# Optimization experiments

Hardware: AMD Instinct MI355X
Metric: run time of the kernel (lower is better)

The kernel has to match this reference:

```python
import jax, jax.numpy as jnp
import numpy as np
from jax import lax

NUM_HEADS = 16
DIM = 1024
BATCH = 4
SEQ = 2048


def setup_inputs() -> dict:
    key = jax.random.key(0)
    ks = jax.random.split(key, 12)
    f32 = jnp.float32
    q = jax.random.normal(ks[0], (BATCH, SEQ, DIM), dtype=f32)
    k = jax.random.normal(ks[1], (BATCH, SEQ, DIM), dtype=f32)
    v = jax.random.normal(ks[2], (BATCH, SEQ, DIM), dtype=f32)
    lim = 1.0 / np.sqrt(DIM)  # nn.Linear default init range
    Wi = jax.random.uniform(ks[3], (DIM, DIM), minval=-lim, maxval=lim, dtype=f32)
    bi = jax.random.uniform(ks[4], (DIM,), minval=-lim, maxval=lim, dtype=f32)
    Wg = jax.random.uniform(ks[5], (DIM, DIM), minval=-lim, maxval=lim, dtype=f32)
    bg = jax.random.uniform(ks[6], (DIM,), minval=-lim, maxval=lim, dtype=f32)
    Wo = jax.random.uniform(ks[7], (DIM, DIM), minval=-lim, maxval=lim, dtype=f32)
    bo = jax.random.uniform(ks[8], (DIM,), minval=-lim, maxval=lim, dtype=f32)
    A = jax.random.normal(ks[9], (DIM, DIM), dtype=f32) * 0.1
    Bm = jax.random.normal(ks[10], (DIM, DIM), dtype=f32) * 0.1
    decay = jnp.full((1, NUM_HEADS, 1), 0.9, dtype=f32)
    return dict(q=q, k=k, v=v, Wi=Wi, bi=bi, Wg=Wg, bg=bg, A=A, Bm=Bm,
                Wo=Wo, bo=bo, decay=decay)


def reference(q, k, v, Wi, bi, Wg, bg, A, Bm, Wo, bo, decay):
    B, S, D = q.shape
    H = decay.shape[1]
    hd = D // H
    # time-major heads: [S, B, H, hd]
    qh = jnp.moveaxis(q.reshape(B, S, H, hd), 1, 0)
    kh = jnp.moveaxis(k.reshape(B, S, H, hd), 1, 0)
    vh = jnp.moveaxis(v.reshape(B, S, H, hd), 1, 0)

    def step(carry, xs):
        r, state = carry
        qt, kt, vt = xs
        r = decay * r + kt * vt                         # [B, H, hd]
        retained = (qt * r).reshape(B, D)               # [B, D]
        inp = retained @ Wi.T + bi
        gate = jax.nn.sigmoid(inp @ Wg.T + bg)
        blended = gate * state + (1.0 - gate) * inp
        state = jnp.tanh(blended @ A.T + inp @ Bm.T)
        out = state @ Wo.T + bo                         # [B, D]
        return (r, state), out

    r0 = jnp.zeros((B, H, hd), dtype=q.dtype)
    s0 = jnp.zeros((B, D), dtype=q.dtype)
    _, outs = lax.scan(step, (r0, s0), (qh, kh, vh))     # outs: [S, B, D]
    return jnp.moveaxis(outs, 0, 1)                      # [B, S, D]
```

## Files before the change

kernel.cpp:

```cpp
#include <hip/hip_runtime.h>
#include <hip/hip_bf16.h>
#include <math.h>

#define BATCH 4
#define SEQ   2048
#define DIM   1024
#define MROWS (SEQ*BATCH)
#define BIGN  ((size_t)MROWS*DIM)

__global__ __launch_bounds__(256) void scan_a(const float* __restrict__ K,
    const float* __restrict__ V, const float* __restrict__ dec_p,
    float* __restrict__ E)
{
  int id  = blockIdx.x*256 + threadIdx.x;
  int c   = id >> 12;
  int rem = id & 4095;
  int b   = rem >> 10;
  int dc  = rem & 1023;
  float dec = dec_p[dc >> 6];
  size_t base = ((size_t)b*SEQ + (size_t)c*32)*DIM + dc;
  float r = 0.f;
  #pragma unroll 4
  for (int i = 0; i < 32; ++i) {
    float kv = K[base + (size_t)i*DIM] * V[base + (size_t)i*DIM];
    r = fmaf(dec, r, kv);
  }
  E[(size_t)c*4096 + rem] = r;
}

__global__ __launch_bounds__(256) void scan_b(const float* __restrict__ E,
    const float* __restrict__ dec_p, float* __restrict__ carry)
{
  int id = blockIdx.x*256 + threadIdx.x;
  int dc = id & 1023;
  float dec = dec_p[dc >> 6];
  float d2 = dec*dec, d4 = d2*d2, d8 = d4*d4, d16 = d8*d8, d32 = d16*d16;
  float r = 0.f;
  #pragma unroll 1
  for (int c = 0; c < 64; ++c) {
    carry[(size_t)c*4096 + id] = r;
    r = fmaf(d32, r, E[(size_t)c*4096 + id]);
  }
}

__global__ __launch_bounds__(256) void scan_c(const float* __restrict__ Q,
    const float* __restrict__ K, const float* __restrict__ V,
    const float* __restrict__ dec_p, const float* __restrict__ carry,
    float* __restrict__ ret)
{
  int id  = blockIdx.x*256 + threadIdx.x;
  int c   = id >> 12;
  int rem = id & 4095;
  int b   = rem >> 10;
  int dc  = rem & 1023;
  float dec = dec_p[dc >> 6];
  size_t base = ((size_t)b*SEQ + (size_t)c*32)*DIM + dc;
  float r = carry[(size_t)c*4096 + rem];
  #pragma unroll 1
  for (int i = 0; i < 32; ++i) {
    int t = c*32 + i;
    float kv = K[base + (size_t)i*DIM] * V[base + (size_t)i*DIM];
    r = fmaf(dec, r, kv);
    ret[((size_t)t*BATCH + b)*DIM + dc] = Q[base + (size_t)i*DIM] * r;
  }
}

#define GM 64
#define GN 64
#define GK 32
#define LDA 68

template<int MODE>
__global__ __launch_bounds__(256) void gemm_k(
    const float* __restrict__ X, const float* __restrict__ W,
    const float* __restrict__ bias, float* __restrict__ C,
    const float* __restrict__ inp, float* __restrict__ u_out,
    float* __restrict__ outf)
{
  __shared__ float Xs[GK][LDA];
  __shared__ float Ws[GK][LDA];
  const int tid = threadIdx.x;
  const int m0 = blockIdx.y * GM;
  const int n0 = blockIdx.x * GN;
  const int tx = tid & 15, ty = tid >> 4;
  float acc[4][4] = {};
  #pragma unroll 1
  for (int kb = 0; kb < DIM; kb += GK) {
    #pragma unroll
    for (int h = 0; h < 2; ++h) {
      int idx = tid + h*256;
      int row = idx >> 3;
      int kc  = (idx & 7) << 2;
      float4 xv = *(const float4*)(X + (size_t)(m0+row)*DIM + kb + kc);
      Xs[kc+0][row] = xv.x; Xs[kc+1][row] = xv.y;
      Xs[kc+2][row] = xv.z; Xs[kc+3][row] = xv.w;
      float4 wv = *(const float4*)(W + (size_t)(n0+row)*DIM + kb + kc);
      Ws[kc+0][row] = wv.x; Ws[kc+1][row] = wv.y;
      Ws[kc+2][row] = wv.z; Ws[kc+3][row] = wv.w;
    }
    __syncthreads();
    #pragma unroll
    for (int kk = 0; kk < GK; ++kk) {
      float4 a = *(const float4*)&Xs[kk][ty << 2];
      float4 w = *(const float4*)&Ws[kk][tx << 2];
      float av[4] = {a.x, a.y, a.z, a.w};
      float wv[4] = {w.x, w.y, w.z, w.w};
      #pragma unroll
      for (int i = 0; i < 4; ++i)
        #pragma unroll
        for (int j = 0; j < 4; ++j)
          acc[i][j] = fmaf(av[i], wv[j], acc[i][j]);
    }
    __syncthreads();
  }
  float bj[4];
  #pragma unroll
  for (int j = 0; j < 4; ++j)
    bj[j] = (MODE == 0 || MODE == 1 || MODE == 3) ? bias[n0 + (tx<<2) + j] : 0.f;
  #pragma unroll
  for (int i = 0; i < 4; ++i) {
    int m = m0 + (ty<<2) + i;
    #pragma unroll
    for (int j = 0; j < 4; ++j) {
      int n = n0 + (tx<<2) + j;
      size_t off = (size_t)m*DIM + n;
      float vv = acc[i][j] + bj[j];
      if (MODE == 2) vv += C[off];
      if (MODE == 1) {
        float gv = 1.f/(1.f + expf(-vv));
        C[off] = gv;
        u_out[off] = (1.f - gv) * inp[off];
      } else if (MODE == 3) {
        outf[((size_t)(m & 3)*SEQ + (size_t)(m >> 2))*DIM + n] = vv;
      } else {
        C[off] = vv;
      }
    }
  }
}

#define RBLK 64

__global__ __launch_bounds__(512, 2) void recur_k(
    const float* __restrict__ A, const float* __restrict__ g,
    const float* __restrict__ dpre, float* __restrict__ s,
    unsigned long long* __restrict__ sf)
{
  __shared__ __align__(16) float xs[8*132 + 4];
  const int tid = threadIdx.x;
  const int w   = tid >> 6;
  const int ln  = tid & 63;
  const int b   = blockIdx.x >> 4;
  const int blk = blockIdx.x & 15;
  const int row = blk*64 + w*8 + (ln >> 3);
  const int ks  = ln & 7;

  const size_t slotstride = (size_t)BATCH*DIM;
  unsigned long long* sfb = sf + (size_t)b*DIM;

  float4 areg[32];
  #pragma unroll
  for (int j = 0; j < 32; ++j)
    areg[j] = *(const float4*)(A + (size_t)row*DIM + ks*128 + 4*j);

  const int xoff = (tid >> 6)*132 + ((2*tid) & 127);

  #pragma unroll 1
  for (int t = 0; t < SEQ; ++t) {
    float2 gv = *(const float2*)(g + ((size_t)t*4 + b)*DIM + 2*tid);
    float dval = (ks == 0) ? dpre[((size_t)t*4 + b)*DIM + row] : 0.f;

    float acc0 = 0.f, acc1 = 0.f, acc2 = 0.f, acc3 = 0.f;
    if (t > 0) {
      unsigned long long* p0 = sfb + (size_t)((t-1)&1)*slotstride + 2*tid;
      const unsigned want = (unsigned)t;
      union { unsigned long long u; unsigned ui[2]; float f[2]; } a0, a1;
      int guard = 0;
      for (;;) {
        a0.u = __hip_atomic_load(p0,     __ATOMIC_RELAXED,
                                 __HIP_MEMORY_SCOPE_AGENT);
        a1.u = __hip_atomic_load(p0 + 1, __ATOMIC_RELAXED,
                                 __HIP_MEMORY_SCOPE_AGENT);
        if ((a0.ui[1] == want && a1.ui[1] == want) || ++guard > (1 << 25))
          break;
      }

      *(float2*)(xs + xoff) = make_float2(gv.x * a0.f[0], gv.y * a1.f[0]);
      __syncthreads();

      const float* xb = xs + ks*132;
      #pragma unroll
      for (int j = 0; j < 32; j += 4) {
        float4 x0 = *(const float4*)(xb + 4*j);
        float4 x1 = *(const float4*)(xb + 4*j + 4);
        float4 x2 = *(const float4*)(xb + 4*j + 8);
        float4 x3 = *(const float4*)(xb + 4*j + 12);
        acc0 = fmaf(areg[j+0].x, x0.x, fmaf(areg[j+0].y, x0.y,
               fmaf(areg[j+0].z, x0.z, fmaf(areg[j+0].w, x0.w, acc0))));
        acc1 = fmaf(areg[j+1].x, x1.x, fmaf(areg[j+1].y, x1.y,
               fmaf(areg[j+1].z, x1.z, fmaf(areg[j+1].w, x1.w, acc1))));
        acc2 = fmaf(areg[j+2].x, x2.x, fmaf(areg[j+2].y, x2.y,
               fmaf(areg[j+2].z, x2.z, fmaf(areg[j+2].w, x2.w, acc2))));
        acc3 = fmaf(areg[j+3].x, x3.x, fmaf(areg[j+3].y, x3.y,
               fmaf(areg[j+3].z, x3.z, fmaf(areg[j+3].w, x3.w, acc3))));
      }
    }
    float sum = (acc0 + acc1) + (acc2 + acc3);
    sum += __shfl_xor(sum, 1, 64);
    sum += __shfl_xor(sum, 2, 64);
    sum += __shfl_xor(sum, 4, 64);
    if (ks == 0) {
      float val = tanhf(sum + dval);
      s[((size_t)t*4 + b)*DIM + row] = val;
      union { unsigned long long u; unsigned ui[2]; float f[2]; } pk;
      pk.f[0] = val; pk.ui[1] = (unsigned)(t + 1);
      __hip_atomic_store(sfb + (size_t)(t & 1)*slotstride + row, pk.u,
                         __ATOMIC_RELAXED, __HIP_MEMORY_SCOPE_AGENT);
    }
    __syncthreads();
  }
}

extern "C" void kernel_launch(void* const* d_in, const int* in_sizes, int n_in,
                              void* d_out, int out_size, void* d_ws, size_t ws_size,
                              hipStream_t stream)
{
  (void)in_sizes; (void)n_in; (void)out_size;
  const float* q   = (const float*)d_in[0];
  const float* k   = (const float*)d_in[1];
  const float* v   = (const float*)d_in[2];
  const float* Wi  = (const float*)d_in[3];
  const float* bi  = (const float*)d_in[4];
  const float* Wg  = (const float*)d_in[5];
  const float* bg  = (const float*)d_in[6];
  const float* A   = (const float*)d_in[7];
  const float* Bm  = (const float*)d_in[8];
  const float* Wo  = (const float*)d_in[9];
  const float* bo  = (const float*)d_in[10];
  const float* dec = (const float*)d_in[11];

  const size_t sf_bytes = (size_t)2*BATCH*DIM*sizeof(unsigned long long);
  size_t need = (4*BIGN + 2*(size_t)64*4096)*sizeof(float) + sf_bytes;
  if (ws_size < need) return;

  float* b0 = (float*)d_ws;
  float* b1 = b0 + BIGN;
  float* b2 = b1 + BIGN;
  float* b3 = b2 + BIGN;
  float* E     = b3 + BIGN;
  float* carry = E + (size_t)64*4096;
  unsigned long long* sf = (unsigned long long*)(carry + (size_t)64*4096);
  float* outp  = (float*)d_out;

  hipMemsetAsync(sf, 0, sf_bytes, stream);

  scan_a<<<1024, 256, 0, stream>>>(k, v, dec, E);
  scan_b<<<16,   256, 0, stream>>>(E, dec, carry);
  scan_c<<<1024, 256, 0, stream>>>(q, k, v, dec, carry, b0);

  dim3 gg(DIM/GN, MROWS/GM);
  gemm_k<0><<<gg, 256, 0, stream>>>(b0, Wi, bi, b1, nullptr, nullptr, nullptr);
  gemm_k<1><<<gg, 256, 0, stream>>>(b1, Wg, bg, b2, b1, b0, nullptr);
  gemm_k<4><<<gg, 256, 0, stream>>>(b0, A,  nullptr, b3, nullptr, nullptr, nullptr);
  gemm_k<2><<<gg, 256, 0, stream>>>(b1, Bm, nullptr, b3, nullptr, nullptr, nullptr);

  recur_k<<<RBLK, 512, 0, stream>>>(A, b2, b3, b0, sf);

  gemm_k<3><<<gg, 256, 0, stream>>>(b0, Wo, bo, nullptr, nullptr, nullptr, outp);
}
```

Measured before the change: 5.460 ms.

## Use packed FP32 FMA in GEMM and recurrence, lighten barriers, publish state earlier

Rewrites the inner products of the tiled GEMM and the sequential recurrence kernel to use two-wide vector FMAs, which the compiler can lower to packed FP32 instructions (v_pk_fma_f32). It replaces __syncthreads in the recurrence loop with raw s_barrier asm, keeping an LDS waitcnt only where one is needed. It also moves the atomic publish of the new state ahead of the plain global store, so other blocks waiting on the serial chain see it sooner. The hand-written barriers give up the compiler's full memory fence, which could allow ordering hazards between the LDS reads and the next iteration's writes.

```diff
diff --git a/kernel.cpp b/kernel.cpp
--- a/kernel.cpp
+++ b/kernel.cpp
@@ -7,6 +7,8 @@
 #define DIM   1024
 #define MROWS (SEQ*BATCH)
 #define BIGN  ((size_t)MROWS*DIM)
+
+typedef float v2f __attribute__((ext_vector_type(2)));
 
 __global__ __launch_bounds__(256) void scan_a(const float* __restrict__ K,
     const float* __restrict__ V, const float* __restrict__ dec_p,
@@ -83,7 +85,7 @@
   const int m0 = blockIdx.y * GM;
   const int n0 = blockIdx.x * GN;
   const int tx = tid & 15, ty = tid >> 4;
-  float acc[4][4] = {};
+  v2f acc[4][2] = {};
   #pragma unroll 1
   for (int kb = 0; kb < DIM; kb += GK) {
     #pragma unroll
@@ -103,13 +105,15 @@
     for (int kk = 0; kk < GK; ++kk) {
       float4 a = *(const float4*)&Xs[kk][ty << 2];
       float4 w = *(const float4*)&Ws[kk][tx << 2];
+      v2f w0 = {w.x, w.y};
+      v2f w1 = {w.z, w.w};
       float av[4] = {a.x, a.y, a.z, a.w};
-      float wv[4] = {w.x, w.y, w.z, w.w};
       #pragma unroll
-      for (int i = 0; i < 4; ++i)
-        #pragma unroll
-        for (int j = 0; j < 4; ++j)
-          acc[i][j] = fmaf(av[i], wv[j], acc[i][j]);
+      for (int i = 0; i < 4; ++i) {
+        v2f ab = {av[i], av[i]};
+        acc[i][0] = __builtin_elementwise_fma(ab, w0, acc[i][0]);
+        acc[i][1] = __builtin_elementwise_fma(ab, w1, acc[i][1]);
+      }
     }
     __syncthreads();
   }
@@ -124,7 +128,7 @@
     for (int j = 0; j < 4; ++j) {
       int n = n0 + (tx<<2) + j;
       size_t off = (size_t)m*DIM + n;
-      float vv = acc[i][j] + bj[j];
+      float vv = acc[i][j >> 1][j & 1] + bj[j];
       if (MODE == 2) vv += C[off];
       if (MODE == 1) {
         float gv = 1.f/(1.f + expf(-vv));
@@ -162,6 +166,7 @@
   #pragma unroll
   for (int j = 0; j < 32; ++j)
     areg[j] = *(const float4*)(A + (size_t)row*DIM + ks*128 + 4*j);
+  const v2f* a2 = reinterpret_cast<const v2f*>(areg);
 
   const int xoff = (tid >> 6)*132 + ((2*tid) & 127);
 
@@ -170,7 +175,8 @@
     float2 gv = *(const float2*)(g + ((size_t)t*4 + b)*DIM + 2*tid);
     float dval = (ks == 0) ? dpre[((size_t)t*4 + b)*DIM + row] : 0.f;
 
-    float acc0 = 0.f, acc1 = 0.f, acc2 = 0.f, acc3 = 0.f;
+    v2f acc0 = {0.f, 0.f}, acc1 = {0.f, 0.f};
+    v2f acc2 = {0.f, 0.f}, acc3 = {0.f, 0.f};
     if (t > 0) {
       unsigned long long* p0 = sfb + (size_t)((t-1)&1)*slotstride + 2*tid;
       const unsigned want = (unsigned)t;
@@ -186,7 +192,7 @@
       }
 
       *(float2*)(xs + xoff) = make_float2(gv.x * a0.f[0], gv.y * a1.f[0]);
-      __syncthreads();
+      asm volatile("s_waitcnt lgkmcnt(0)\n\ts_barrier" ::: "memory");
 
       const float* xb = xs + ks*132;
       #pragma unroll
@@ -195,29 +201,34 @@
         float4 x1 = *(const float4*)(xb + 4*j + 4);
         float4 x2 = *(const float4*)(xb + 4*j + 8);
         float4 x3 = *(const float4*)(xb + 4*j + 12);
-        acc0 = fmaf(areg[j+0].x, x0.x, fmaf(areg[j+0].y, x0.y,
-               fmaf(areg[j+0].z, x0.z, fmaf(areg[j+0].w, x0.w, acc0))));
-        acc1 = fmaf(areg[j+1].x, x1.x, fmaf(areg[j+1].y, x1.y,
-               fmaf(areg[j+1].z, x1.z, fmaf(areg[j+1].w, x1.w, acc1))));
-        acc2 = fmaf(areg[j+2].x, x2.x, fmaf(areg[j+2].y, x2.y,
-               fmaf(areg[j+2].z, x2.z, fmaf(areg[j+2].w, x2.w, acc2))));
-        acc3 = fmaf(areg[j+3].x, x3.x, fmaf(areg[j+3].y, x3.y,
-               fmaf(areg[j+3].z, x3.z, fmaf(areg[j+3].w, x3.w, acc3))));
-      }
-    }
-    float sum = (acc0 + acc1) + (acc2 + acc3);
+        v2f x0l = {x0.x, x0.y}, x0h = {x0.z, x0.w};
+        v2f x1l = {x1.x, x1.y}, x1h = {x1.z, x1.w};
+        v2f x2l = {x2.x, x2.y}, x2h = {x2.z, x2.w};
+        v2f x3l = {x3.x, x3.y}, x3h = {x3.z, x3.w};
+        acc0 = __builtin_elementwise_fma(a2[2*j+0], x0l, acc0);
+        acc0 = __builtin_elementwise_fma(a2[2*j+1], x0h, acc0);
+        acc1 = __builtin_elementwise_fma(a2[2*j+2], x1l, acc1);
+        acc1 = __builtin_elementwise_fma(a2[2*j+3], x1h, acc1);
+        acc2 = __builtin_elementwise_fma(a2[2*j+4], x2l, acc2);
+        acc2 = __builtin_elementwise_fma(a2[2*j+5], x2h, acc2);
+        acc3 = __builtin_elementwise_fma(a2[2*j+6], x3l, acc3);
+        acc3 = __builtin_elementwise_fma(a2[2*j+7], x3h, acc3);
+      }
+    }
+    v2f accp = (acc0 + acc1) + (acc2 + acc3);
+    float sum = accp.x + accp.y;
     sum += __shfl_xor(sum, 1, 64);
     sum += __shfl_xor(sum, 2, 64);
     sum += __shfl_xor(sum, 4, 64);
     if (ks == 0) {
       float val = tanhf(sum + dval);
-      s[((size_t)t*4 + b)*DIM + row] = val;
       union { unsigned long long u; unsigned ui[2]; float f[2]; } pk;
       pk.f[0] = val; pk.ui[1] = (unsigned)(t + 1);
       __hip_atomic_store(sfb + (size_t)(t & 1)*slotstride + row, pk.u,
                          __ATOMIC_RELAXED, __HIP_MEMORY_SCOPE_AGENT);
-    }
-    __syncthreads();
+      s[((size_t)t*4 + b)*DIM + row] = val;
+    }
+    asm volatile("s_barrier" ::: "memory");
   }
 }
 
```

Result: faster. 5.078 ms (-7.0%).
